# Kernel optimization log

Measured on AMD Instinct MI355X. Metric: run time of the kernel, lower is better.

The kernel has to match this reference:

```python
import jax, jax.numpy as jnp
import numpy as np

B = 4096
INPUT_SIZE = 1024
HIDDEN_SIZE = 1024


def setup_inputs() -> dict:
    key = jax.random.key(0)
    ks = jax.random.split(key, 11)
    f32 = jnp.float32
    inp = {
        "x_t": jax.random.normal(ks[0], (B, INPUT_SIZE), dtype=f32),
        "h_prev": jax.random.normal(ks[1], (B, HIDDEN_SIZE), dtype=f32),
        "c_prev": jax.random.normal(ks[2], (B, HIDDEN_SIZE), dtype=f32),
        "W_f": jax.random.normal(ks[3], (INPUT_SIZE, HIDDEN_SIZE), dtype=f32),
        "W_i": jax.random.normal(ks[4], (INPUT_SIZE, HIDDEN_SIZE), dtype=f32),
        "W_c": jax.random.normal(ks[5], (INPUT_SIZE, HIDDEN_SIZE), dtype=f32),
        "W_o": jax.random.normal(ks[6], (INPUT_SIZE, HIDDEN_SIZE), dtype=f32),
        "U_f": jax.random.normal(ks[7], (HIDDEN_SIZE, HIDDEN_SIZE), dtype=f32),
        "U_i": jax.random.normal(ks[8], (HIDDEN_SIZE, HIDDEN_SIZE), dtype=f32),
        "U_c": jax.random.normal(ks[9], (HIDDEN_SIZE, HIDDEN_SIZE), dtype=f32),
        "U_o": jax.random.normal(ks[10], (HIDDEN_SIZE, HIDDEN_SIZE), dtype=f32),
        "b_f": jnp.zeros((HIDDEN_SIZE,), dtype=f32),
        "b_i": jnp.zeros((HIDDEN_SIZE,), dtype=f32),
        "b_c": jnp.zeros((HIDDEN_SIZE,), dtype=f32),
        "b_o": jnp.zeros((HIDDEN_SIZE,), dtype=f32),
    }
    return inp


def reference(x_t, h_prev, c_prev,
              W_f, W_i, W_c, W_o,
              U_f, U_i, U_c, U_o,
              b_f, b_i, b_c, b_o):
    # Fuse the 8 small GEMMs into 2 big ones by concatenating gate weights.
    W = jnp.concatenate([W_f, W_i, W_c, W_o], axis=1)  # [I, 4H]
    U = jnp.concatenate([U_f, U_i, U_c, U_o], axis=1)  # [H, 4H]
    b = jnp.concatenate([b_f, b_i, b_c, b_o], axis=0)  # [4H]
    gates = x_t @ W + h_prev @ U + b                    # [B, 4H]
    H = h_prev.shape[-1]
    f_t = jax.nn.sigmoid(gates[:, 0 * H:1 * H])
    i_t = jax.nn.sigmoid(gates[:, 1 * H:2 * H])
    c_tilda_t = jnp.tanh(gates[:, 2 * H:3 * H])
    o_t = jax.nn.sigmoid(gates[:, 3 * H:4 * H])
    c_t = f_t * c_prev + i_t * c_tilda_t
    h_t = o_t * jnp.tanh(c_t)
    return h_t
```

## Files before the change

kernel.cpp:

```cpp
#include <hip/hip_runtime.h>

typedef unsigned short u16;
typedef __attribute__((ext_vector_type(8))) short bf16x8;
typedef __attribute__((ext_vector_type(4))) float f32x4;

#define HID 1024
#define BATCH 4096
#define K3 6144
#define NGATE 4096
#define BK 32
#define NT 192

__device__ __forceinline__ u16 f2bf(float f) {
  unsigned int u = __float_as_uint(f);
  u += 0x7FFFu + ((u >> 16) & 1u);
  return (u16)(u >> 16);
}
__device__ __forceinline__ float bf2f(u16 h) {
  return __uint_as_float(((unsigned int)h) << 16);
}

__device__ __forceinline__ void load16_to_lds(const void* g, void* l) {
  __builtin_amdgcn_global_load_lds(
      (const __attribute__((address_space(1))) unsigned int*)g,
      (__attribute__((address_space(3))) unsigned int*)l, 16, 0, 0);
}

__device__ __forceinline__ float sigmoid_f(float x) {
  return 1.f / (1.f + __expf(-x));
}
__device__ __forceinline__ float tanh_f(float x) {
  return 1.f - 2.f / (__expf(2.f * x) + 1.f);
}

__global__ void pack_act(const float* __restrict__ x, const float* __restrict__ h,
                         u16* __restrict__ Bt) {
  size_t idx = (size_t)blockIdx.x * 256 + threadIdx.x;
  int m  = (int)(idx >> 9);
  int kq = (int)(idx & 511) << 2;
  const float* src = (kq < 1024) ? (x + (size_t)m * 1024 + kq)
                                 : (h + (size_t)m * 1024 + (kq - 1024));
  float4 v = *(const float4*)src;
  ushort4 hi, lo;
  hi.x = f2bf(v.x); lo.x = f2bf(v.x - bf2f(hi.x));
  hi.y = f2bf(v.y); lo.y = f2bf(v.y - bf2f(hi.y));
  hi.z = f2bf(v.z); lo.z = f2bf(v.z - bf2f(hi.z));
  hi.w = f2bf(v.w); lo.w = f2bf(v.w - bf2f(hi.w));
  u16* row = Bt + (size_t)m * K3;
  *(ushort4*)(row + kq)        = hi;
  *(ushort4*)(row + 2048 + kq) = lo;
  *(ushort4*)(row + 4096 + kq) = hi;
}

__global__ void pack_w(const float* __restrict__ Wf, const float* __restrict__ Wi,
                       const float* __restrict__ Wc, const float* __restrict__ Wo,
                       const float* __restrict__ Uf, const float* __restrict__ Ui,
                       const float* __restrict__ Uc, const float* __restrict__ Uo,
                       u16* __restrict__ P) {
  __shared__ float ldsT[32][33];
  int bid = blockIdx.x;
  int mat = bid >> 10;
  int tid = bid & 1023;
  int k0 = (tid >> 5) << 5;
  int h0 = (tid & 31) << 5;
  int g = mat & 3;
  const float* S;
  {
    const float* a = (mat & 1) ? ((mat & 2) ? Wo : Wi) : ((mat & 2) ? Wc : Wf);
    const float* b = (mat & 1) ? ((mat & 2) ? Uo : Ui) : ((mat & 2) ? Uc : Uf);
    S = (mat & 4) ? b : a;
  }
  int kbase = (mat & 4) ? 1024 : 0;

  int t = threadIdx.x;
  {
    int r0 = t >> 5;
    int c  = t & 31;
#pragma unroll
    for (int j = 0; j < 4; ++j)
      ldsT[c][r0 + 8 * j] = S[(size_t)(k0 + r0 + 8 * j) * 1024 + h0 + c];
  }
  __syncthreads();
  {
    int c  = t >> 3;
    int kq = (t & 7) << 2;
    int n  = ((h0 + c) << 2) + g;
    float v0 = ldsT[c][kq + 0], v1 = ldsT[c][kq + 1];
    float v2 = ldsT[c][kq + 2], v3 = ldsT[c][kq + 3];
    ushort4 hi, lo;
    hi.x = f2bf(v0); lo.x = f2bf(v0 - bf2f(hi.x));
    hi.y = f2bf(v1); lo.y = f2bf(v1 - bf2f(hi.y));
    hi.z = f2bf(v2); lo.z = f2bf(v2 - bf2f(hi.z));
    hi.w = f2bf(v3); lo.w = f2bf(v3 - bf2f(hi.w));
    u16* base = P + (size_t)n * K3 + kbase + k0 + kq;
    *(ushort4*)(base)        = hi;
    *(ushort4*)(base + 2048) = hi;
    *(ushort4*)(base + 4096) = lo;
  }
}

__global__ void pack_bias(const float* __restrict__ bf, const float* __restrict__ bi,
                          const float* __restrict__ bc, const float* __restrict__ bo,
                          float* __restrict__ bcat) {
  int i = blockIdx.x * 256 + threadIdx.x;
  if (i < NGATE) {
    int h = i >> 2, g = i & 3;
    const float* b = (g == 0) ? bf : (g == 1) ? bi : (g == 2) ? bc : bo;
    bcat[i] = b[h];
  }
}

__global__ __launch_bounds__(512, 2) void lstm_gemm(
    const u16* __restrict__ P, const u16* __restrict__ Bt,
    const float* __restrict__ bcat, const float* __restrict__ c_prev,
    float* __restrict__ out) {
  __shared__ __align__(16) u16 As[4][256 * BK];
  __shared__ __align__(16) u16 Bs[4][256 * BK];

  const int t = threadIdx.x;
  const int w = t >> 6;
  const int l = t & 63;

  const int bid = blockIdx.x;
  const int swz = ((bid & 7) << 5) + (bid >> 3);
  const int n0 = (swz & 15) << 8;
  const int m0 = (swz >> 4) << 8;

  const int wm = w >> 2;
  const int wn = w & 3;

  const int srow = t >> 2;
  const int ssl  = (((t & 3) ^ ((srow >> 1) & 3)) << 3);
  const u16* gA0 = P  + (size_t)(n0 + srow)       * K3 + ssl;
  const u16* gA1 = P  + (size_t)(n0 + 128 + srow) * K3 + ssl;
  const u16* gB0 = Bt + (size_t)(m0 + srow)       * K3 + ssl;
  const u16* gB1 = Bt + (size_t)(m0 + 128 + srow) * K3 + ssl;
  const int ldw0 = w << 9;
  const int ldw1 = 4096 + (w << 9);

  const int fr = l & 15;
  const int sl = l >> 4;
  int offA[8], offB[4];
#pragma unroll
  for (int i = 0; i < 8; ++i) {
    int ar = (wm << 7) + i * 16 + fr;
    offA[i] = ar * BK + ((sl ^ ((ar >> 1) & 3)) << 3);
  }
#pragma unroll
  for (int j = 0; j < 4; ++j) {
    int br = (wn << 6) + j * 16 + fr;
    offB[j] = br * BK + ((sl ^ ((br >> 1) & 3)) << 3);
  }

  f32x4 acc[8][4];
#pragma unroll
  for (int i = 0; i < 8; ++i)
#pragma unroll
    for (int j = 0; j < 4; ++j) acc[i][j] = (f32x4){0.f, 0.f, 0.f, 0.f};

#pragma unroll
  for (int pt = 0; pt < 3; ++pt) {
    const int kt = pt * BK;
    load16_to_lds(gA0 + kt, &As[pt][ldw0]);
    load16_to_lds(gA1 + kt, &As[pt][ldw1]);
    load16_to_lds(gB0 + kt, &Bs[pt][ldw0]);
    load16_to_lds(gB1 + kt, &Bs[pt][ldw1]);
  }

  for (int t4 = 0; t4 < NT; t4 += 4) {
#pragma unroll
    for (int u = 0; u < 4; ++u) {
      const int tt  = t4 + u;
      const int pfi = tt + 3;
      const int pkt = (pfi < NT ? pfi : NT - 1) * BK;
      const int pc  = (u + 3) & 3;

      asm volatile("s_waitcnt lgkmcnt(0)" ::: "memory");
      asm volatile("s_waitcnt vmcnt(8)" ::: "memory");
      __builtin_amdgcn_s_barrier();
      __builtin_amdgcn_sched_barrier(0);

      load16_to_lds(gA0 + pkt, &As[pc][ldw0]);
      load16_to_lds(gA1 + pkt, &As[pc][ldw1]);
      load16_to_lds(gB0 + pkt, &Bs[pc][ldw0]);
      load16_to_lds(gB1 + pkt, &Bs[pc][ldw1]);

      bf16x8 aF[4], aG[4], bF[4];
#pragma unroll
      for (int i = 0; i < 4; ++i) aF[i] = *(const bf16x8*)&As[u][offA[i]];
#pragma unroll
      for (int j = 0; j < 4; ++j) bF[j] = *(const bf16x8*)&Bs[u][offB[j]];
#pragma unroll
      for (int i = 0; i < 4; ++i) aG[i] = *(const bf16x8*)&As[u][offA[4 + i]];

      __builtin_amdgcn_s_setprio(1);
#pragma unroll
      for (int i = 0; i < 4; ++i)
#pragma unroll
        for (int j = 0; j < 4; ++j)
          acc[i][j] = __builtin_amdgcn_mfma_f32_16x16x32_bf16(aF[i], bF[j], acc[i][j], 0, 0, 0);
#pragma unroll
      for (int i = 0; i < 4; ++i)
#pragma unroll
        for (int j = 0; j < 4; ++j)
          acc[4 + i][j] = __builtin_amdgcn_mfma_f32_16x16x32_bf16(aG[i], bF[j], acc[4 + i][j], 0, 0, 0);
      __builtin_amdgcn_s_setprio(0);
    }
  }

  const int n_base = n0 + (wm << 7);
  const int m_base = m0 + (wn << 6);
#pragma unroll
  for (int i = 0; i < 8; ++i) {
    int nf = n_base + i * 16 + ((l >> 4) << 2);
    int hq = nf >> 2;
    float4 b4 = *(const float4*)&bcat[nf];
#pragma unroll
    for (int j = 0; j < 4; ++j) {
      int m = m_base + j * 16 + fr;
      f32x4 a = acc[i][j];
      float ft = sigmoid_f(a[0] + b4.x);
      float it = sigmoid_f(a[1] + b4.y);
      float ct = tanh_f   (a[2] + b4.z);
      float ot = sigmoid_f(a[3] + b4.w);
      float cp = c_prev[(size_t)m * HID + hq];
      float cn = ft * cp + it * ct;
      out[(size_t)m * HID + hq] = ot * tanh_f(cn);
    }
  }
}

extern "C" void kernel_launch(void* const* d_in, const int* in_sizes, int n_in,
                              void* d_out, int out_size, void* d_ws, size_t ws_size,
                              hipStream_t stream) {
  const float* x  = (const float*)d_in[0];
  const float* hp = (const float*)d_in[1];
  const float* cp = (const float*)d_in[2];
  const float* Wf = (const float*)d_in[3];
  const float* Wi = (const float*)d_in[4];
  const float* Wc = (const float*)d_in[5];
  const float* Wo = (const float*)d_in[6];
  const float* Uf = (const float*)d_in[7];
  const float* Ui = (const float*)d_in[8];
  const float* Uc = (const float*)d_in[9];
  const float* Uo = (const float*)d_in[10];
  const float* bf = (const float*)d_in[11];
  const float* bi = (const float*)d_in[12];
  const float* bc = (const float*)d_in[13];
  const float* bo = (const float*)d_in[14];

  const size_t P_BYTES  = (size_t)NGATE * K3 * 2;
  const size_t BT_BYTES = (size_t)BATCH * K3 * 2;
  u16*   Pw   = (u16*)d_ws;
  u16*   Bt   = (u16*)((char*)d_ws + P_BYTES);
  float* bcat = (float*)((char*)d_ws + P_BYTES + BT_BYTES);
  float* out  = (float*)d_out;

  pack_act <<<dim3(8192), dim3(256), 0, stream>>>(x, hp, Bt);
  pack_w   <<<dim3(8192), dim3(256), 0, stream>>>(Wf, Wi, Wc, Wo, Uf, Ui, Uc, Uo, Pw);
  pack_bias<<<dim3(16),   dim3(256), 0, stream>>>(bf, bi, bc, bo, bcat);
  lstm_gemm<<<dim3(256),  dim3(512), 0, stream>>>(Pw, Bt, bcat, cp, out);
}
```

Baseline: 223.7 us.

## Shrink GEMM block tile to 256x128 with triple buffering for more blocks

Halves the batch dimension of each block tile (256 gate columns by 128 batch rows), so each warp computes a 64x64 tile instead of 128x64. The grid doubles to 512 blocks and the LDS pipeline goes from four stages to three, with launch bounds raised so more blocks can reside per CU. The goal is better occupancy and balance across the 256 CUs, since 256 blocks give only one wave of work. The cost is less operand reuse per block, which means more global and LDS traffic per FLOP, plus a shallower prefetch depth.

```diff
diff --git a/kernel.cpp b/kernel.cpp
--- a/kernel.cpp
+++ b/kernel.cpp
@@ -110,88 +110,83 @@
   }
 }
 
-__global__ __launch_bounds__(512, 2) void lstm_gemm(
+__global__ __launch_bounds__(512, 4) void lstm_gemm(
     const u16* __restrict__ P, const u16* __restrict__ Bt,
     const float* __restrict__ bcat, const float* __restrict__ c_prev,
     float* __restrict__ out) {
-  __shared__ __align__(16) u16 As[4][256 * BK];
-  __shared__ __align__(16) u16 Bs[4][256 * BK];
+  __shared__ __align__(16) u16 As[3][256 * BK];
+  __shared__ __align__(16) u16 Bs[3][128 * BK];
 
   const int t = threadIdx.x;
   const int w = t >> 6;
   const int l = t & 63;
 
   const int bid = blockIdx.x;
-  const int swz = ((bid & 7) << 5) + (bid >> 3);
-  const int n0 = (swz & 15) << 8;
-  const int m0 = (swz >> 4) << 8;
-
+  const int swz = ((bid & 7) << 6) + (bid >> 3);
+  const int n0 = (swz >> 5) << 8;
+  const int m0 = (swz & 31) << 7;
+
+  const int wn = w & 3;
   const int wm = w >> 2;
-  const int wn = w & 3;
 
   const int srow = t >> 2;
   const int ssl  = (((t & 3) ^ ((srow >> 1) & 3)) << 3);
   const u16* gA0 = P  + (size_t)(n0 + srow)       * K3 + ssl;
   const u16* gA1 = P  + (size_t)(n0 + 128 + srow) * K3 + ssl;
   const u16* gB0 = Bt + (size_t)(m0 + srow)       * K3 + ssl;
-  const u16* gB1 = Bt + (size_t)(m0 + 128 + srow) * K3 + ssl;
   const int ldw0 = w << 9;
   const int ldw1 = 4096 + (w << 9);
 
   const int fr = l & 15;
   const int sl = l >> 4;
-  int offA[8], offB[4];
-#pragma unroll
-  for (int i = 0; i < 8; ++i) {
-    int ar = (wm << 7) + i * 16 + fr;
+  int offA[4], offB[4];
+#pragma unroll
+  for (int i = 0; i < 4; ++i) {
+    int ar = (wn << 6) + i * 16 + fr;
     offA[i] = ar * BK + ((sl ^ ((ar >> 1) & 3)) << 3);
   }
 #pragma unroll
   for (int j = 0; j < 4; ++j) {
-    int br = (wn << 6) + j * 16 + fr;
+    int br = (wm << 6) + j * 16 + fr;
     offB[j] = br * BK + ((sl ^ ((br >> 1) & 3)) << 3);
   }
 
-  f32x4 acc[8][4];
-#pragma unroll
-  for (int i = 0; i < 8; ++i)
+  f32x4 acc[4][4];
+#pragma unroll
+  for (int i = 0; i < 4; ++i)
 #pragma unroll
     for (int j = 0; j < 4; ++j) acc[i][j] = (f32x4){0.f, 0.f, 0.f, 0.f};
 
 #pragma unroll
-  for (int pt = 0; pt < 3; ++pt) {
+  for (int pt = 0; pt < 2; ++pt) {
     const int kt = pt * BK;
     load16_to_lds(gA0 + kt, &As[pt][ldw0]);
     load16_to_lds(gA1 + kt, &As[pt][ldw1]);
     load16_to_lds(gB0 + kt, &Bs[pt][ldw0]);
-    load16_to_lds(gB1 + kt, &Bs[pt][ldw1]);
-  }
-
-  for (int t4 = 0; t4 < NT; t4 += 4) {
-#pragma unroll
-    for (int u = 0; u < 4; ++u) {
-      const int tt  = t4 + u;
-      const int pfi = tt + 3;
+  }
+
+  for (int t3 = 0; t3 < NT; t3 += 3) {
+#pragma unroll
+    for (int u = 0; u < 3; ++u) {
+      const int tt  = t3 + u;
+      const int pfi = tt + 2;
       const int pkt = (pfi < NT ? pfi : NT - 1) * BK;
-      const int pc  = (u + 3) & 3;
+      const int pc  = (u + 2) % 3;
 
       asm volatile("s_waitcnt lgkmcnt(0)" ::: "memory");
-      asm volatile("s_waitcnt vmcnt(8)" ::: "memory");
+      asm volatile("s_waitcnt vmcnt(3)" ::: "memory");
       __builtin_amdgcn_s_barrier();
       __builtin_amdgcn_sched_barrier(0);
 
       load16_to_lds(gA0 + pkt, &As[pc][ldw0]);
       load16_to_lds(gA1 + pkt, &As[pc][ldw1]);
       load16_to_lds(gB0 + pkt, &Bs[pc][ldw0]);
-      load16_to_lds(gB1 + pkt, &Bs[pc][ldw1]);
-
-      bf16x8 aF[4], aG[4], bF[4];
+
+      bf16x8 aF[4], bF[4];
 #pragma unroll
       for (int i = 0; i < 4; ++i) aF[i] = *(const bf16x8*)&As[u][offA[i]];
 #pragma unroll
       for (int j = 0; j < 4; ++j) bF[j] = *(const bf16x8*)&Bs[u][offB[j]];
-#pragma unroll
-      for (int i = 0; i < 4; ++i) aG[i] = *(const bf16x8*)&As[u][offA[4 + i]];
 
       __builtin_amdgcn_s_setprio(1);
 #pragma unroll
@@ -199,19 +194,14 @@
 #pragma unroll
         for (int j = 0; j < 4; ++j)
           acc[i][j] = __builtin_amdgcn_mfma_f32_16x16x32_bf16(aF[i], bF[j], acc[i][j], 0, 0, 0);
-#pragma unroll
-      for (int i = 0; i < 4; ++i)
-#pragma unroll
-        for (int j = 0; j < 4; ++j)
-          acc[4 + i][j] = __builtin_amdgcn_mfma_f32_16x16x32_bf16(aG[i], bF[j], acc[4 + i][j], 0, 0, 0);
       __builtin_amdgcn_s_setprio(0);
     }
   }
 
-  const int n_base = n0 + (wm << 7);
-  const int m_base = m0 + (wn << 6);
-#pragma unroll
-  for (int i = 0; i < 8; ++i) {
+  const int n_base = n0 + (wn << 6);
+  const int m_base = m0 + (wm << 6);
+#pragma unroll
+  for (int i = 0; i < 4; ++i) {
     int nf = n_base + i * 16 + ((l >> 4) << 2);
     int hq = nf >> 2;
     float4 b4 = *(const float4*)&bcat[nf];
@@ -259,5 +249,5 @@
   pack_act <<<dim3(8192), dim3(256), 0, stream>>>(x, hp, Bt);
   pack_w   <<<dim3(8192), dim3(256), 0, stream>>>(Wf, Wi, Wc, Wo, Uf, Ui, Uc, Uo, Pw);
   pack_bias<<<dim3(16),   dim3(256), 0, stream>>>(bf, bi, bc, bo, bcat);
-  lstm_gemm<<<dim3(256),  dim3(512), 0, stream>>>(Pw, Bt, bcat, cp, out);
-}
+  lstm_gemm<<<dim3(512),  dim3(512), 0, stream>>>(Pw, Bt, bcat, cp, out);
+}
```

After: 252.6 us. 1.13x slower.

## Switch GEMM main loop to double-buffered BK=64 tiles with half the barriers

Applied to the files above, without the earlier changes.

The GEMM main loop changes from a 4-stage ring of BK=32 tiles, prefetched 3 ahead with a partial vmcnt wait, to 2 buffers of BK=64 tiles, each split into two 32-wide halves, prefetched one tile ahead with a full vmcnt(0) wait. This halves the number of barrier and waitcnt points per K and doubles the MFMA work between syncs. The cost is a shallower prefetch: each iteration waits for all outstanding loads, so global latency may be less hidden. LDS footprint stays the same.

```diff
diff --git a/kernel.cpp b/kernel.cpp
--- a/kernel.cpp
+++ b/kernel.cpp
@@ -8,8 +8,8 @@
 #define BATCH 4096
 #define K3 6144
 #define NGATE 4096
-#define BK 32
-#define NT 192
+#define BK 64
+#define NT 96
 
 __device__ __forceinline__ u16 f2bf(float f) {
   unsigned int u = __float_as_uint(f);
@@ -114,8 +114,8 @@
     const u16* __restrict__ P, const u16* __restrict__ Bt,
     const float* __restrict__ bcat, const float* __restrict__ c_prev,
     float* __restrict__ out) {
-  __shared__ __align__(16) u16 As[4][256 * BK];
-  __shared__ __align__(16) u16 Bs[4][256 * BK];
+  __shared__ __align__(16) u16 As[2][2][8192];
+  __shared__ __align__(16) u16 Bs[2][2][8192];
 
   const int t = threadIdx.x;
   const int w = t >> 6;
@@ -131,12 +131,9 @@
 
   const int srow = t >> 2;
   const int ssl  = (((t & 3) ^ ((srow >> 1) & 3)) << 3);
-  const u16* gA0 = P  + (size_t)(n0 + srow)       * K3 + ssl;
-  const u16* gA1 = P  + (size_t)(n0 + 128 + srow) * K3 + ssl;
-  const u16* gB0 = Bt + (size_t)(m0 + srow)       * K3 + ssl;
-  const u16* gB1 = Bt + (size_t)(m0 + 128 + srow) * K3 + ssl;
-  const int ldw0 = w << 9;
-  const int ldw1 = 4096 + (w << 9);
+  const u16* gA = P  + (size_t)(n0 + srow) * K3 + ssl;
+  const u16* gB = Bt + (size_t)(m0 + srow) * K3 + ssl;
+  const int dq = w << 9;
 
   const int fr = l & 15;
   const int sl = l >> 4;
@@ -144,12 +141,12 @@
 #pragma unroll
   for (int i = 0; i < 8; ++i) {
     int ar = (wm << 7) + i * 16 + fr;
-    offA[i] = ar * BK + ((sl ^ ((ar >> 1) & 3)) << 3);
+    offA[i] = ar * 32 + ((sl ^ ((ar >> 1) & 3)) << 3);
   }
 #pragma unroll
   for (int j = 0; j < 4; ++j) {
     int br = (wn << 6) + j * 16 + fr;
-    offB[j] = br * BK + ((sl ^ ((br >> 1) & 3)) << 3);
+    offB[j] = br * 32 + ((sl ^ ((br >> 1) & 3)) << 3);
   }
 
   f32x4 acc[8][4];
@@ -158,53 +155,79 @@
 #pragma unroll
     for (int j = 0; j < 4; ++j) acc[i][j] = (f32x4){0.f, 0.f, 0.f, 0.f};
 
-#pragma unroll
-  for (int pt = 0; pt < 3; ++pt) {
-    const int kt = pt * BK;
-    load16_to_lds(gA0 + kt, &As[pt][ldw0]);
-    load16_to_lds(gA1 + kt, &As[pt][ldw1]);
-    load16_to_lds(gB0 + kt, &Bs[pt][ldw0]);
-    load16_to_lds(gB1 + kt, &Bs[pt][ldw1]);
-  }
-
-  for (int t4 = 0; t4 < NT; t4 += 4) {
-#pragma unroll
-    for (int u = 0; u < 4; ++u) {
-      const int tt  = t4 + u;
-      const int pfi = tt + 3;
-      const int pkt = (pfi < NT ? pfi : NT - 1) * BK;
-      const int pc  = (u + 3) & 3;
+  load16_to_lds(gA,                         &As[0][0][dq]);
+  load16_to_lds(gA + (size_t)128 * K3,      &As[0][0][dq + 4096]);
+  load16_to_lds(gB,                         &Bs[0][0][dq]);
+  load16_to_lds(gB + (size_t)128 * K3,      &Bs[0][0][dq + 4096]);
+  load16_to_lds(gA + 32,                    &As[0][1][dq]);
+  load16_to_lds(gA + 32 + (size_t)128 * K3, &As[0][1][dq + 4096]);
+  load16_to_lds(gB + 32,                    &Bs[0][1][dq]);
+  load16_to_lds(gB + 32 + (size_t)128 * K3, &Bs[0][1][dq + 4096]);
+
+  for (int T2 = 0; T2 < NT; T2 += 2) {
+#pragma unroll
+    for (int u = 0; u < 2; ++u) {
+      const int T  = T2 + u;
+      const int pf = (T + 1 < NT) ? T + 1 : NT - 1;
+      const size_t pfk = (size_t)pf * BK;
+      const int nb = u ^ 1;
 
       asm volatile("s_waitcnt lgkmcnt(0)" ::: "memory");
-      asm volatile("s_waitcnt vmcnt(8)" ::: "memory");
+      asm volatile("s_waitcnt vmcnt(0)" ::: "memory");
       __builtin_amdgcn_s_barrier();
       __builtin_amdgcn_sched_barrier(0);
 
-      load16_to_lds(gA0 + pkt, &As[pc][ldw0]);
-      load16_to_lds(gA1 + pkt, &As[pc][ldw1]);
-      load16_to_lds(gB0 + pkt, &Bs[pc][ldw0]);
-      load16_to_lds(gB1 + pkt, &Bs[pc][ldw1]);
-
-      bf16x8 aF[4], aG[4], bF[4];
-#pragma unroll
-      for (int i = 0; i < 4; ++i) aF[i] = *(const bf16x8*)&As[u][offA[i]];
-#pragma unroll
-      for (int j = 0; j < 4; ++j) bF[j] = *(const bf16x8*)&Bs[u][offB[j]];
-#pragma unroll
-      for (int i = 0; i < 4; ++i) aG[i] = *(const bf16x8*)&As[u][offA[4 + i]];
-
-      __builtin_amdgcn_s_setprio(1);
-#pragma unroll
-      for (int i = 0; i < 4; ++i)
-#pragma unroll
-        for (int j = 0; j < 4; ++j)
-          acc[i][j] = __builtin_amdgcn_mfma_f32_16x16x32_bf16(aF[i], bF[j], acc[i][j], 0, 0, 0);
-#pragma unroll
-      for (int i = 0; i < 4; ++i)
-#pragma unroll
-        for (int j = 0; j < 4; ++j)
-          acc[4 + i][j] = __builtin_amdgcn_mfma_f32_16x16x32_bf16(aG[i], bF[j], acc[4 + i][j], 0, 0, 0);
-      __builtin_amdgcn_s_setprio(0);
+      load16_to_lds(gA + pfk,                         &As[nb][0][dq]);
+      load16_to_lds(gA + pfk + (size_t)128 * K3,      &As[nb][0][dq + 4096]);
+      load16_to_lds(gB + pfk,                         &Bs[nb][0][dq]);
+      load16_to_lds(gB + pfk + (size_t)128 * K3,      &Bs[nb][0][dq + 4096]);
+      load16_to_lds(gA + pfk + 32,                    &As[nb][1][dq]);
+      load16_to_lds(gA + pfk + 32 + (size_t)128 * K3, &As[nb][1][dq + 4096]);
+      load16_to_lds(gB + pfk + 32,                    &Bs[nb][1][dq]);
+      load16_to_lds(gB + pfk + 32 + (size_t)128 * K3, &Bs[nb][1][dq + 4096]);
+
+      {
+        bf16x8 aF[4], aG[4], bF[4];
+#pragma unroll
+        for (int i = 0; i < 4; ++i) aF[i] = *(const bf16x8*)&As[u][0][offA[i]];
+#pragma unroll
+        for (int j = 0; j < 4; ++j) bF[j] = *(const bf16x8*)&Bs[u][0][offB[j]];
+#pragma unroll
+        for (int i = 0; i < 4; ++i) aG[i] = *(const bf16x8*)&As[u][0][offA[4 + i]];
+        __builtin_amdgcn_s_setprio(1);
+#pragma unroll
+        for (int i = 0; i < 4; ++i)
+#pragma unroll
+          for (int j = 0; j < 4; ++j)
+            acc[i][j] = __builtin_amdgcn_mfma_f32_16x16x32_bf16(aF[i], bF[j], acc[i][j], 0, 0, 0);
+#pragma unroll
+        for (int i = 0; i < 4; ++i)
+#pragma unroll
+          for (int j = 0; j < 4; ++j)
+            acc[4 + i][j] = __builtin_amdgcn_mfma_f32_16x16x32_bf16(aG[i], bF[j], acc[4 + i][j], 0, 0, 0);
+        __builtin_amdgcn_s_setprio(0);
+      }
+      {
+        bf16x8 aF[4], aG[4], bF[4];
+#pragma unroll
+        for (int i = 0; i < 4; ++i) aF[i] = *(const bf16x8*)&As[u][1][offA[i]];
+#pragma unroll
+        for (int j = 0; j < 4; ++j) bF[j] = *(const bf16x8*)&Bs[u][1][offB[j]];
+#pragma unroll
+        for (int i = 0; i < 4; ++i) aG[i] = *(const bf16x8*)&As[u][1][offA[4 + i]];
+        __builtin_amdgcn_s_setprio(1);
+#pragma unroll
+        for (int i = 0; i < 4; ++i)
+#pragma unroll
+          for (int j = 0; j < 4; ++j)
+            acc[i][j] = __builtin_amdgcn_mfma_f32_16x16x32_bf16(aF[i], bF[j], acc[i][j], 0, 0, 0);
+#pragma unroll
+        for (int i = 0; i < 4; ++i)
+#pragma unroll
+          for (int j = 0; j < 4; ++j)
+            acc[4 + i][j] = __builtin_amdgcn_mfma_f32_16x16x32_bf16(aG[i], bF[j], acc[4 + i][j], 0, 0, 0);
+        __builtin_amdgcn_s_setprio(0);
+      }
     }
   }
 
```

After: 227.7 us. Within noise of the previous version (+1.8%).
